# Optimization experiments

Measured on AMD Instinct MI355X. Metric: run time of the kernel, lower is better.

## Reference

```python
import jax, jax.numpy as jnp
import numpy as np

NUM_HEADS = 16


def setup_inputs() -> dict:
    key = jax.random.key(0)
    ks = jax.random.split(key, 11)
    S, E, F = 4096, 2048, 8192
    s = lambda k, shape, fan_in: jax.random.normal(k, shape, jnp.float32) / np.sqrt(fan_in)
    return {
        "emb": jax.random.normal(ks[0], (S, E), jnp.float32),
        "Wq": s(ks[1], (E, E), E), "bq": jnp.zeros((E,), jnp.float32),
        "Wk": s(ks[2], (E, E), E), "bk": jnp.zeros((E,), jnp.float32),
        "Wv": s(ks[3], (E, E), E), "bv": jnp.zeros((E,), jnp.float32),
        "W1": s(ks[4], (E, F), E), "b1": jnp.zeros((F,), jnp.float32),
        "W2": s(ks[5], (F, E), F), "b2": jnp.zeros((E,), jnp.float32),
    }


def reference(emb, Wq, bq, Wk, bk, Wv, bv, W1, b1, W2, b2):
    S, E = emb.shape
    H = NUM_HEADS
    D = E // H
    # project and split heads -> [H, S, D]
    q = (emb @ Wq + bq).reshape(S, H, D).transpose(1, 0, 2)
    k = (emb @ Wk + bk).reshape(S, H, D).transpose(1, 0, 2)
    v = (emb @ Wv + bv).reshape(S, H, D).transpose(1, 0, 2)
    scale = jnp.asarray(D, emb.dtype) ** 0.5
    scores = jnp.einsum("hsd,htd->hst", q, k) / scale  # [H, S, S]
    # causal mask: additive -1e9 strictly above the diagonal (matches torch.triu(..., 1)*-1e9)
    mask = jnp.triu(jnp.full((S, S), -1e9, dtype=scores.dtype), k=1)
    probs = jax.nn.softmax(scores + mask, axis=-1)
    attn = jnp.einsum("hst,htd->hsd", probs, v)  # [H, S, D]
    attn = attn.transpose(1, 0, 2).reshape(S, E)  # concat heads -> [S, E]
    hidden = jnp.maximum(attn @ W1 + b1, 0.0)
    return hidden @ W2 + b2
```

## Files before the change

kernel.cpp:

```cpp
#include <hip/hip_runtime.h>

typedef __attribute__((ext_vector_type(8))) short bf16x8;
typedef __attribute__((ext_vector_type(4))) float f32x4;

static constexpr int S = 4096;
static constexpr int E = 2048;
static constexpr int F = 8192;
static constexpr int NH = 16;
static constexpr int DH = 128;

__device__ __forceinline__ unsigned short f2bf(float f) {
  unsigned u = __builtin_bit_cast(unsigned, f);
  u += 0x7FFFu + ((u >> 16) & 1u);
  return (unsigned short)(u >> 16);
}

__device__ __forceinline__ void async16(const unsigned short* g, unsigned short* l) {
  __builtin_amdgcn_global_load_lds(
      (const __attribute__((address_space(1))) unsigned int*)g,
      (__attribute__((address_space(3))) unsigned int*)l, 16, 0, 0);
}

#define BARRIER() asm volatile("s_barrier" ::: "memory")
#define WAIT_VM(n) asm volatile("s_waitcnt vmcnt(" #n ")" ::: "memory")
#define LGKM0() asm volatile("s_waitcnt lgkmcnt(0)" ::: "memory")

__global__ __launch_bounds__(256) void cvt_bf16_kernel(const float* __restrict__ src,
                                                       unsigned short* __restrict__ dst) {
  int i = (blockIdx.x * 256 + threadIdx.x) * 4;
  float4 v = *(const float4*)(src + i);
  ushort4 o;
  o.x = f2bf(v.x); o.y = f2bf(v.y); o.z = f2bf(v.z); o.w = f2bf(v.w);
  *(ushort4*)(dst + i) = o;
}

__global__ __launch_bounds__(256) void transpose_cvt(const float* __restrict__ src,
                                                     unsigned short* __restrict__ dst,
                                                     const int Rr, const int Cc) {
  __shared__ float t[64][65];
  const int c0 = blockIdx.x * 64, r0 = blockIdx.y * 64;
  const int tid = threadIdx.x;
  const int lx = tid & 15, ly = tid >> 4;
#pragma unroll
  for (int p = 0; p < 4; ++p) {
    const int r = p * 16 + ly;
    const float4 v = *(const float4*)(src + (size_t)(r0 + r) * Cc + c0 + lx * 4);
    t[r][lx * 4 + 0] = v.x; t[r][lx * 4 + 1] = v.y;
    t[r][lx * 4 + 2] = v.z; t[r][lx * 4 + 3] = v.w;
  }
  __syncthreads();
#pragma unroll
  for (int p = 0; p < 4; ++p) {
    const int c = p * 16 + ly;
    ushort4 o;
    o.x = f2bf(t[lx * 4 + 0][c]);
    o.y = f2bf(t[lx * 4 + 1][c]);
    o.z = f2bf(t[lx * 4 + 2][c]);
    o.w = f2bf(t[lx * 4 + 3][c]);
    *(ushort4*)(dst + (size_t)(c0 + c) * Rr + r0 + lx * 4) = o;
  }
}

enum { EPI_QKV = 0, EPI_RELU = 1, EPI_OUT = 2 };

template <int EPI>
__global__ __launch_bounds__(256) void gemm_bt(
    const unsigned short* __restrict__ A, const unsigned short* __restrict__ B,
    const int K, const int N,
    const float* __restrict__ b0, const float* __restrict__ b1f, const float* __restrict__ b2f,
    unsigned short* __restrict__ o0, unsigned short* __restrict__ o1,
    unsigned short* __restrict__ o2, float* __restrict__ of) {
  __shared__ unsigned short lA[2][128 * 32];
  __shared__ unsigned short lB[2][128 * 32];
  const int tid = threadIdx.x, w = tid >> 6, lane = tid & 63;
  const int lane15 = lane & 15, l4 = lane >> 4;
  const int m0 = blockIdx.y * 128, n0 = blockIdx.x * 128;
  const int wr = w >> 1, wc = w & 1;

  const int u0 = (w * 2 + 0) * 64 + lane;
  const int u1 = (w * 2 + 1) * 64 + lane;
  const unsigned short* gA0 = A + (size_t)(m0 + (u0 >> 2)) * K + (u0 & 3) * 8;
  const unsigned short* gA1 = A + (size_t)(m0 + (u1 >> 2)) * K + (u1 & 3) * 8;
  const unsigned short* gB0 = B + (size_t)(n0 + (u0 >> 2)) * K + (u0 & 3) * 8;
  const unsigned short* gB1 = B + (size_t)(n0 + (u1 >> 2)) * K + (u1 & 3) * 8;
  const int doff0 = (w * 2 + 0) * 512;
  const int doff1 = (w * 2 + 1) * 512;

  f32x4 zero4 = {0.f, 0.f, 0.f, 0.f};
  f32x4 acc[4][4];
#pragma unroll
  for (int i = 0; i < 4; ++i)
#pragma unroll
    for (int j = 0; j < 4; ++j) acc[i][j] = zero4;

  async16(gA0, &lA[0][doff0]);
  async16(gA1, &lA[0][doff1]);
  async16(gB0, &lB[0][doff0]);
  async16(gB1, &lB[0][doff1]);

  for (int ko = 0; ko < K; ko += 32) {
    __syncthreads();
    const int buf = (ko >> 5) & 1;
    if (ko + 32 < K) {
      const int nb = buf ^ 1;
      async16(gA0 + ko + 32, &lA[nb][doff0]);
      async16(gA1 + ko + 32, &lA[nb][doff1]);
      async16(gB0 + ko + 32, &lB[nb][doff0]);
      async16(gB1 + ko + 32, &lB[nb][doff1]);
    }
    bf16x8 av[4], bv[4];
#pragma unroll
    for (int i = 0; i < 4; ++i)
      av[i] = *(const bf16x8*)&lA[buf][(wr * 64 + i * 16 + lane15) * 32 + l4 * 8];
#pragma unroll
    for (int j = 0; j < 4; ++j)
      bv[j] = *(const bf16x8*)&lB[buf][(wc * 64 + j * 16 + lane15) * 32 + l4 * 8];
#pragma unroll
    for (int i = 0; i < 4; ++i)
#pragma unroll
      for (int j = 0; j < 4; ++j)
        acc[i][j] = __builtin_amdgcn_mfma_f32_16x16x32_bf16(av[i], bv[j], acc[i][j], 0, 0, 0);
  }

#pragma unroll
  for (int j = 0; j < 4; ++j) {
    const int n = n0 + wc * 64 + j * 16 + lane15;
    float bias;
    if (EPI == EPI_QKV)
      bias = (n < E) ? b0[n] : ((n < 2 * E) ? b1f[n - E] : b2f[n - 2 * E]);
    else
      bias = b0[n];
#pragma unroll
    for (int i = 0; i < 4; ++i) {
      const int mr = m0 + wr * 64 + i * 16 + l4 * 4;
      f32x4 v = acc[i][j];
#pragma unroll
      for (int r = 0; r < 4; ++r) {
        const float val = v[r] + bias;
        const int m = mr + r;
        if (EPI == EPI_QKV) {
          if (n < E)            o0[(size_t)m * E + n] = f2bf(val);
          else if (n < 2 * E)   o1[(size_t)m * E + (n - E)] = f2bf(val);
          else                  o2[(size_t)(n - 2 * E) * S + m] = f2bf(val);
        } else if (EPI == EPI_RELU) {
          o0[(size_t)m * N + n] = f2bf(fmaxf(val, 0.f));
        } else {
          of[(size_t)m * N + n] = val;
        }
      }
    }
  }
}

template <int EPI>
__global__ __launch_bounds__(512, 1) void gemm8(
    const unsigned short* __restrict__ A, const unsigned short* __restrict__ B,
    const int K, const int N,
    const float* __restrict__ b0,
    unsigned short* __restrict__ o0, float* __restrict__ of) {
  __shared__ unsigned short lA[2][256 * 64];
  __shared__ unsigned short lB[2][256 * 64];
  const int tid = threadIdx.x, w = tid >> 6, lane = tid & 63;
  const int lane15 = lane & 15, l4 = lane >> 4;
  const int wr = w >> 2, wc = w & 3;

  const int gx = gridDim.x, gy = gridDim.y;
  const int hw = blockIdx.y * gx + blockIdx.x;
  const int chunk = (gx * gy) >> 3;
  const int pos = (hw & 7) * chunk + (hw >> 3);
  const int bx = pos / gy, by = pos % gy;
  const int m0 = by * 256, n0 = bx * 256;

  const int prow = tid >> 3;
  const int pcc = (tid & 7) ^ (prow & 7);
  const unsigned short* gA = A + (size_t)(m0 + prow) * K + pcc * 8;
  const unsigned short* gB = B + (size_t)(n0 + prow) * K + pcc * 8;
  const size_t rstep = (size_t)64 * K;
  const int lw = w * 512;

  const int pswz0 = l4 ^ (lane15 & 7);
  const int pswz1 = (4 + l4) ^ (lane15 & 7);
  const int arow = (wr * 128 + lane15) * 64;
  const int brow = (wc * 64 + lane15) * 64;

  f32x4 zero4 = {0.f, 0.f, 0.f, 0.f};
  f32x4 acc[8][4];
#pragma unroll
  for (int i = 0; i < 8; ++i)
#pragma unroll
    for (int j = 0; j < 4; ++j) acc[i][j] = zero4;

#pragma unroll
  for (int r = 0; r < 4; ++r) async16(gB + r * rstep, &lB[0][r * 4096 + lw]);
#pragma unroll
  for (int r = 0; r < 4; ++r) async16(gA + r * rstep, &lA[0][r * 4096 + lw]);
  WAIT_VM(0);
  BARRIER();

  const int NT = K >> 6;
  bf16x8 a0[4][2], bb0[2][2], bb1[2][2];
  for (int t = 0; t < NT; ++t) {
    const unsigned short* lAb = lA[t & 1];
    const unsigned short* lBb = lB[t & 1];
    unsigned short* lAn = lA[(t & 1) ^ 1];
    unsigned short* lBn = lB[(t & 1) ^ 1];
    const size_t ko = (size_t)(t + 1) * 64;
    const bool nxt = (t + 1 < NT);

#pragma unroll
    for (int mi = 0; mi < 4; ++mi) {
      a0[mi][0] = *(const bf16x8*)&lAb[arow + mi * 1024 + pswz0 * 8];
      a0[mi][1] = *(const bf16x8*)&lAb[arow + mi * 1024 + pswz1 * 8];
    }
#pragma unroll
    for (int nj = 0; nj < 2; ++nj) {
      bb0[nj][0] = *(const bf16x8*)&lBb[brow + nj * 1024 + pswz0 * 8];
      bb0[nj][1] = *(const bf16x8*)&lBb[brow + nj * 1024 + pswz1 * 8];
    }
    if (nxt) {
      async16(gB + 0 * rstep + ko, &lBn[0 * 4096 + lw]);
      async16(gB + 1 * rstep + ko, &lBn[1 * 4096 + lw]);
    }
    BARRIER();
    LGKM0();
    __builtin_amdgcn_s_setprio(1);
#pragma unroll
    for (int mi = 0; mi < 4; ++mi)
#pragma unroll
      for (int nj = 0; nj < 2; ++nj)
#pragma unroll
        for (int kk = 0; kk < 2; ++kk)
          acc[mi][nj] = __builtin_amdgcn_mfma_f32_16x16x32_bf16(a0[mi][kk], bb0[nj][kk], acc[mi][nj], 0, 0, 0);
    __builtin_amdgcn_s_setprio(0);
    BARRIER();

#pragma unroll
    for (int nj = 0; nj < 2; ++nj) {
      bb1[nj][0] = *(const bf16x8*)&lBb[brow + 2048 + nj * 1024 + pswz0 * 8];
      bb1[nj][1] = *(const bf16x8*)&lBb[brow + 2048 + nj * 1024 + pswz1 * 8];
    }
    if (nxt) {
      async16(gB + 2 * rstep + ko, &lBn[2 * 4096 + lw]);
      async16(gB + 3 * rstep + ko, &lBn[3 * 4096 + lw]);
    }
    BARRIER();
    LGKM0();
    __builtin_amdgcn_s_setprio(1);
#pragma unroll
    for (int mi = 0; mi < 4; ++mi)
#pragma unroll
      for (int nj = 0; nj < 2; ++nj)
#pragma unroll
        for (int kk = 0; kk < 2; ++kk)
          acc[mi][2 + nj] = __builtin_amdgcn_mfma_f32_16x16x32_bf16(a0[mi][kk], bb1[nj][kk], acc[mi][2 + nj], 0, 0, 0);
    __builtin_amdgcn_s_setprio(0);
    if (nxt)
      WAIT_VM(4);
    else
      WAIT_VM(0);
    BARRIER();

#pragma unroll
    for (int mi = 0; mi < 4; ++mi) {
      a0[mi][0] = *(const bf16x8*)&lAb[arow + 4096 + mi * 1024 + pswz0 * 8];
      a0[mi][1] = *(const bf16x8*)&lAb[arow + 4096 + mi * 1024 + pswz1 * 8];
    }
    if (nxt) {
      async16(gA + 0 * rstep + ko, &lAn[0 * 4096 + lw]);
      async16(gA + 2 * rstep + ko, &lAn[2 * 4096 + lw]);
    }
    BARRIER();
    LGKM0();
    __builtin_amdgcn_s_setprio(1);
#pragma unroll
    for (int mi = 0; mi < 4; ++mi)
#pragma unroll
      for (int nj = 0; nj < 2; ++nj)
#pragma unroll
        for (int kk = 0; kk < 2; ++kk)
          acc[4 + mi][2 + nj] = __builtin_amdgcn_mfma_f32_16x16x32_bf16(a0[mi][kk], bb1[nj][kk], acc[4 + mi][2 + nj], 0, 0, 0);
    __builtin_amdgcn_s_setprio(0);
    BARRIER();

    if (nxt) {
      async16(gA + 1 * rstep + ko, &lAn[1 * 4096 + lw]);
      async16(gA + 3 * rstep + ko, &lAn[3 * 4096 + lw]);
    }
    BARRIER();
    __builtin_amdgcn_s_setprio(1);
#pragma unroll
    for (int mi = 0; mi < 4; ++mi)
#pragma unroll
      for (int nj = 0; nj < 2; ++nj)
#pragma unroll
        for (int kk = 0; kk < 2; ++kk)
          acc[4 + mi][nj] = __builtin_amdgcn_mfma_f32_16x16x32_bf16(a0[mi][kk], bb0[nj][kk], acc[4 + mi][nj], 0, 0, 0);
    __builtin_amdgcn_s_setprio(0);
    if (nxt)
      WAIT_VM(2);
    BARRIER();
  }

#pragma unroll
  for (int j = 0; j < 4; ++j) {
    const int n = n0 + wc * 64 + j * 16 + lane15;
    const float bias = b0[n];
#pragma unroll
    for (int i = 0; i < 8; ++i) {
      const int mr = m0 + wr * 128 + i * 16 + l4 * 4;
      f32x4 v = acc[i][j];
#pragma unroll
      for (int r = 0; r < 4; ++r) {
        const float val = v[r] + bias;
        const int m = mr + r;
        if (EPI == EPI_RELU) {
          o0[(size_t)m * N + n] = f2bf(fmaxf(val, 0.f));
        } else {
          of[(size_t)m * N + n] = val;
        }
      }
    }
  }
}

__global__ __launch_bounds__(256, 2) void flash_attn(const unsigned short* __restrict__ Qb,
                                                     const unsigned short* __restrict__ Kb,
                                                     const unsigned short* __restrict__ VTb,
                                                     unsigned short* __restrict__ attn) {
  const int x = blockIdx.x;
  const int h = blockIdx.y;
  const int qt = (h < 8) ? (31 - x) : x;
  const int qbase = qt * 128;
  const int tid = threadIdx.x, w = tid >> 6, lane = tid & 63;
  const int lane15 = lane & 15, l4 = lane >> 4;
  const int rowb = qbase + w * 32;

  __shared__ unsigned short lK[2][64 * 128];
  __shared__ unsigned short lV[2][128 * 64];
  __shared__ unsigned short lP[4][16 * 72];

  bf16x8 aq[2][4];
#pragma unroll
  for (int rg = 0; rg < 2; ++rg) {
    const unsigned short* qrow = Qb + (size_t)(rowb + rg * 16 + lane15) * E + h * DH + l4 * 8;
#pragma unroll
    for (int kk = 0; kk < 4; ++kk) aq[rg][kk] = *(const bf16x8*)(qrow + kk * 32);
  }

  f32x4 zero4 = {0.f, 0.f, 0.f, 0.f};
  f32x4 o[2][8];
  float psum[2][4];
#pragma unroll
  for (int rg = 0; rg < 2; ++rg) {
#pragma unroll
    for (int j = 0; j < 8; ++j) o[rg][j] = zero4;
#pragma unroll
    for (int r = 0; r < 4; ++r) psum[rg][r] = 0.f;
  }

  {
#pragma unroll
    for (int i = 0; i < 4; ++i) {
      int c = i * 256 + w * 64 + lane;
      int row = c >> 4, pg = (c & 15) ^ (row & 15);
      async16(Kb + (size_t)row * E + h * DH + pg * 8, &lK[0][(i * 256 + w * 64) * 8]);
    }
#pragma unroll
    for (int i = 0; i < 4; ++i) {
      int c = i * 256 + w * 64 + lane;
      int row = c >> 3, pg = (c & 7) ^ (row & 7);
      async16(VTb + (size_t)(h * DH + row) * S + pg * 8, &lV[0][(i * 256 + w * 64) * 8]);
    }
  }

  const float scale = 0.088388347648318447f;
  const int ktmax = 2 * qt + 1;

  for (int kt = 0; kt <= ktmax; ++kt) {
    __syncthreads();
    if (kt < ktmax) {
      const int kb2 = (kt + 1) * 64;
      const int nb = (kt + 1) & 1;
#pragma unroll
      for (int i = 0; i < 4; ++i) {
        int c = i * 256 + w * 64 + lane;
        int row = c >> 4, pg = (c & 15) ^ (row & 15);
        async16(Kb + (size_t)(kb2 + row) * E + h * DH + pg * 8, &lK[nb][(i * 256 + w * 64) * 8]);
      }
#pragma unroll
      for (int i = 0; i < 4; ++i) {
        int c = i * 256 + w * 64 + lane;
        int row = c >> 3, pg = (c & 7) ^ (row & 7);
        async16(VTb + (size_t)(h * DH + row) * S + kb2 + pg * 8, &lV[nb][(i * 256 + w * 64) * 8]);
      }
    }
    if (kt * 64 > rowb + 31) continue;
    const int buf = kt & 1;

    f32x4 sacc[2][4];
#pragma unroll
    for (int rg = 0; rg < 2; ++rg)
#pragma unroll
      for (int j = 0; j < 4; ++j) sacc[rg][j] = zero4;
#pragma unroll
    for (int kk = 0; kk < 4; ++kk)
#pragma unroll
      for (int j = 0; j < 4; ++j) {
        int pl = (kk * 4 + l4) ^ lane15;
        bf16x8 bk = *(const bf16x8*)&lK[buf][(j * 16 + lane15) * 128 + pl * 8];
        sacc[0][j] = __builtin_amdgcn_mfma_f32_16x16x32_bf16(aq[0][kk], bk, sacc[0][j], 0, 0, 0);
        sacc[1][j] = __builtin_amdgcn_mfma_f32_16x16x32_bf16(aq[1][kk], bk, sacc[1][j], 0, 0, 0);
      }

    const bool diag = (kt * 64 + 63 > rowb);
    bf16x8 ap[2][2];
#pragma unroll
    for (int rg = 0; rg < 2; ++rg) {
      float p[4][4];
      if (diag) {
#pragma unroll
        for (int j = 0; j < 4; ++j) {
          int col = kt * 64 + j * 16 + lane15;
#pragma unroll
          for (int r = 0; r < 4; ++r) {
            int row = rowb + rg * 16 + l4 * 4 + r;
            p[j][r] = (col <= row) ? __expf(sacc[rg][j][r] * scale) : 0.f;
          }
        }
      } else {
#pragma unroll
        for (int j = 0; j < 4; ++j)
#pragma unroll
          for (int r = 0; r < 4; ++r) p[j][r] = __expf(sacc[rg][j][r] * scale);
      }
#pragma unroll
      for (int r = 0; r < 4; ++r) psum[rg][r] += p[0][r] + p[1][r] + p[2][r] + p[3][r];

#pragma unroll
      for (int j = 0; j < 4; ++j)
#pragma unroll
        for (int r = 0; r < 4; ++r)
          lP[w][(l4 * 4 + r) * 72 + j * 16 + lane15] = f2bf(p[j][r]);

#pragma unroll
      for (int ks = 0; ks < 2; ++ks)
        ap[rg][ks] = *(const bf16x8*)&lP[w][lane15 * 72 + ks * 32 + l4 * 8];
    }

#pragma unroll
    for (int ks = 0; ks < 2; ++ks)
#pragma unroll
      for (int j = 0; j < 8; ++j) {
        int pl = (ks * 4 + l4) ^ (lane15 & 7);
        bf16x8 bv = *(const bf16x8*)&lV[buf][(j * 16 + lane15) * 64 + pl * 8];
        o[0][j] = __builtin_amdgcn_mfma_f32_16x16x32_bf16(ap[0][ks], bv, o[0][j], 0, 0, 0);
        o[1][j] = __builtin_amdgcn_mfma_f32_16x16x32_bf16(ap[1][ks], bv, o[1][j], 0, 0, 0);
      }
  }

#pragma unroll
  for (int rg = 0; rg < 2; ++rg) {
    float inv[4];
#pragma unroll
    for (int r = 0; r < 4; ++r) {
      float s = psum[rg][r];
#pragma unroll
      for (int off = 1; off < 16; off <<= 1) s += __shfl_xor(s, off, 16);
      inv[r] = 1.0f / s;
    }
#pragma unroll
    for (int j = 0; j < 8; ++j)
#pragma unroll
      for (int r = 0; r < 4; ++r)
        attn[(size_t)(rowb + rg * 16 + l4 * 4 + r) * E + h * DH + j * 16 + lane15] =
            f2bf(o[rg][j][r] * inv[r]);
  }
}

extern "C" void kernel_launch(void* const* d_in, const int* in_sizes, int n_in,
                              void* d_out, int out_size, void* d_ws, size_t ws_size,
                              hipStream_t stream) {
  (void)in_sizes; (void)n_in; (void)out_size; (void)ws_size;
  const float* emb = (const float*)d_in[0];
  const float* Wq  = (const float*)d_in[1];
  const float* bq  = (const float*)d_in[2];
  const float* Wk  = (const float*)d_in[3];
  const float* bk  = (const float*)d_in[4];
  const float* Wv  = (const float*)d_in[5];
  const float* bv  = (const float*)d_in[6];
  const float* W1  = (const float*)d_in[7];
  const float* b1  = (const float*)d_in[8];
  const float* W2  = (const float*)d_in[9];
  const float* b2  = (const float*)d_in[10];
  float* out = (float*)d_out;

  char* ws = (char*)d_ws;
  const size_t MB = 1024ull * 1024ull;
  unsigned short* embb   = (unsigned short*)(ws);
  unsigned short* attn   = embb;
  char* r1 = ws + 16 * MB;
  unsigned short* WqkvT  = (unsigned short*)(r1);
  unsigned short* Qb     = (unsigned short*)(r1 + 24 * MB);
  unsigned short* Kb     = (unsigned short*)(r1 + 40 * MB);
  unsigned short* VTb    = (unsigned short*)(r1 + 56 * MB);
  unsigned short* hidden = (unsigned short*)(r1);
  unsigned short* W1T    = (unsigned short*)(r1 + 72 * MB);
  unsigned short* W2T    = (unsigned short*)(r1 + 104 * MB);

  dim3 b256(256);
  dim3 b512(512);
  cvt_bf16_kernel<<<dim3((S * E) / 1024), b256, 0, stream>>>(emb, embb);
  transpose_cvt<<<dim3(E / 64, E / 64), b256, 0, stream>>>(Wq, WqkvT, E, E);
  transpose_cvt<<<dim3(E / 64, E / 64), b256, 0, stream>>>(Wk, WqkvT + (size_t)E * E, E, E);
  transpose_cvt<<<dim3(E / 64, E / 64), b256, 0, stream>>>(Wv, WqkvT + 2ull * E * E, E, E);
  transpose_cvt<<<dim3(F / 64, E / 64), b256, 0, stream>>>(W1, W1T, E, F);
  transpose_cvt<<<dim3(E / 64, F / 64), b256, 0, stream>>>(W2, W2T, F, E);

  gemm_bt<EPI_QKV><<<dim3(3 * E / 128, S / 128), b256, 0, stream>>>(
      embb, WqkvT, E, 3 * E, bq, bk, bv, Qb, Kb, VTb, nullptr);
  flash_attn<<<dim3(S / 128, NH), b256, 0, stream>>>(Qb, Kb, VTb, attn);
  gemm8<EPI_RELU><<<dim3(F / 256, S / 256), b512, 0, stream>>>(
      attn, W1T, E, F, b1, hidden, nullptr);
  gemm_bt<EPI_OUT><<<dim3(E / 128, S / 128), b256, 0, stream>>>(
      hidden, W2T, F, E, b2, nullptr, nullptr, nullptr, nullptr, nullptr, out);
}
```

Measured before the change: 839.7 us.

## Prefetch first half of B tile two iterations ahead in GEMM pipeline

Reorders the async global-to-LDS loads in the GEMM main loop so the first two B row-chunks for iteration t+2 are issued into the current buffer once they have been consumed, while the rest of the t+1 loads shift earlier in the iteration. The prologue also issues the first B chunks for the second tile, and the vmcnt waits are retuned to match. The goal is a deeper prefetch that hides more global-memory latency behind MFMA work. The cost is more complex wait-count bookkeeping, with a risk of LDS overwrite hazards if a count is wrong.

New measurement: 838.0 us. Within noise of the previous version (-0.2%).

```diff
diff --git a/kernel.cpp b/kernel.cpp
--- a/kernel.cpp
+++ b/kernel.cpp
@@ -190,22 +190,28 @@
 #pragma unroll
     for (int j = 0; j < 4; ++j) acc[i][j] = zero4;
 
+  const int NT = K >> 6;
+
 #pragma unroll
   for (int r = 0; r < 4; ++r) async16(gB + r * rstep, &lB[0][r * 4096 + lw]);
 #pragma unroll
   for (int r = 0; r < 4; ++r) async16(gA + r * rstep, &lA[0][r * 4096 + lw]);
-  WAIT_VM(0);
+  async16(gB + 0 * rstep + 64, &lB[1][0 * 4096 + lw]);
+  async16(gB + 1 * rstep + 64, &lB[1][1 * 4096 + lw]);
+  WAIT_VM(2);
   BARRIER();
 
-  const int NT = K >> 6;
   bf16x8 a0[4][2], bb0[2][2], bb1[2][2];
   for (int t = 0; t < NT; ++t) {
     const unsigned short* lAb = lA[t & 1];
     const unsigned short* lBb = lB[t & 1];
     unsigned short* lAn = lA[(t & 1) ^ 1];
     unsigned short* lBn = lB[(t & 1) ^ 1];
-    const size_t ko = (size_t)(t + 1) * 64;
-    const bool nxt = (t + 1 < NT);
+    unsigned short* lBc = lB[t & 1];
+    const size_t ko1 = (size_t)(t + 1) * 64;
+    const size_t ko2 = (size_t)(t + 2) * 64;
+    const bool p1 = (t + 1 < NT);
+    const bool p2 = (t + 2 < NT);
 
 #pragma unroll
     for (int mi = 0; mi < 4; ++mi) {
@@ -217,9 +223,9 @@
       bb0[nj][0] = *(const bf16x8*)&lBb[brow + nj * 1024 + pswz0 * 8];
       bb0[nj][1] = *(const bf16x8*)&lBb[brow + nj * 1024 + pswz1 * 8];
     }
-    if (nxt) {
-      async16(gB + 0 * rstep + ko, &lBn[0 * 4096 + lw]);
-      async16(gB + 1 * rstep + ko, &lBn[1 * 4096 + lw]);
+    if (p1) {
+      async16(gB + 2 * rstep + ko1, &lBn[2 * 4096 + lw]);
+      async16(gB + 3 * rstep + ko1, &lBn[3 * 4096 + lw]);
     }
     BARRIER();
     LGKM0();
@@ -239,9 +245,9 @@
       bb1[nj][0] = *(const bf16x8*)&lBb[brow + 2048 + nj * 1024 + pswz0 * 8];
       bb1[nj][1] = *(const bf16x8*)&lBb[brow + 2048 + nj * 1024 + pswz1 * 8];
     }
-    if (nxt) {
-      async16(gB + 2 * rstep + ko, &lBn[2 * 4096 + lw]);
-      async16(gB + 3 * rstep + ko, &lBn[3 * 4096 + lw]);
+    if (p1) {
+      async16(gA + 0 * rstep + ko1, &lAn[0 * 4096 + lw]);
+      async16(gA + 2 * rstep + ko1, &lAn[2 * 4096 + lw]);
     }
     BARRIER();
     LGKM0();
@@ -254,8 +260,8 @@
         for (int kk = 0; kk < 2; ++kk)
           acc[mi][2 + nj] = __builtin_amdgcn_mfma_f32_16x16x32_bf16(a0[mi][kk], bb1[nj][kk], acc[mi][2 + nj], 0, 0, 0);
     __builtin_amdgcn_s_setprio(0);
-    if (nxt)
-      WAIT_VM(4);
+    if (p1)
+      WAIT_VM(6);
     else
       WAIT_VM(0);
     BARRIER();
@@ -265,9 +271,9 @@
       a0[mi][0] = *(const bf16x8*)&lAb[arow + 4096 + mi * 1024 + pswz0 * 8];
       a0[mi][1] = *(const bf16x8*)&lAb[arow + 4096 + mi * 1024 + pswz1 * 8];
     }
-    if (nxt) {
-      async16(gA + 0 * rstep + ko, &lAn[0 * 4096 + lw]);
-      async16(gA + 2 * rstep + ko, &lAn[2 * 4096 + lw]);
+    if (p1) {
+      async16(gA + 1 * rstep + ko1, &lAn[1 * 4096 + lw]);
+      async16(gA + 3 * rstep + ko1, &lAn[3 * 4096 + lw]);
     }
     BARRIER();
     LGKM0();
@@ -282,9 +288,9 @@
     __builtin_amdgcn_s_setprio(0);
     BARRIER();
 
-    if (nxt) {
-      async16(gA + 1 * rstep + ko, &lAn[1 * 4096 + lw]);
-      async16(gA + 3 * rstep + ko, &lAn[3 * 4096 + lw]);
+    if (p2) {
+      async16(gB + 0 * rstep + ko2, &lBc[0 * 4096 + lw]);
+      async16(gB + 1 * rstep + ko2, &lBc[1 * 4096 + lw]);
     }
     BARRIER();
     __builtin_amdgcn_s_setprio(1);
@@ -296,8 +302,12 @@
         for (int kk = 0; kk < 2; ++kk)
           acc[4 + mi][nj] = __builtin_amdgcn_mfma_f32_16x16x32_bf16(a0[mi][kk], bb0[nj][kk], acc[4 + mi][nj], 0, 0, 0);
     __builtin_amdgcn_s_setprio(0);
-    if (nxt)
+    if (p2)
+      WAIT_VM(4);
+    else if (p1)
       WAIT_VM(2);
+    else
+      WAIT_VM(0);
     BARRIER();
   }
 
```
